# Optimization experiments

Measured on AMD Instinct MI355X. Metric: run time of the kernel, lower is better.

## Reference

```python
import jax, jax.numpy as jnp
import numpy as np

N_NODES = 20000
N_EDGES = 320000
F_IN = 256      # num_features_mol
HIDDEN = 512    # hidden_size


def _glorot(key, shape):
    fan_in, fan_out = shape
    lim = jnp.sqrt(6.0 / (fan_in + fan_out)).astype(jnp.float32)
    return jax.random.uniform(key, shape, jnp.float32, -lim, lim)


def setup_inputs() -> dict:
    key = jax.random.key(0)
    ks = jax.random.split(key, 12)
    x = jax.random.normal(ks[0], (N_NODES, F_IN), jnp.float32)
    edge_index = jax.random.randint(ks[1], (2, N_EDGES), 0, N_NODES, dtype=jnp.int64)
    d1, d2, d3 = F_IN * 2, F_IN * 2, F_IN * 4  # 512, 512, 1024
    return {
        "x": x,
        "edge_index": edge_index,
        # SAGEConv layer i: lin_l (neighbor, with bias), lin_r (root, no bias)
        "Wl1": _glorot(ks[2], (F_IN, d1)), "bl1": jnp.zeros((d1,), jnp.float32),
        "Wr1": _glorot(ks[3], (F_IN, d1)),
        "Wl2": _glorot(ks[4], (d1, d2)), "bl2": jnp.zeros((d2,), jnp.float32),
        "Wr2": _glorot(ks[5], (d1, d2)),
        "Wl3": _glorot(ks[6], (d2, d3)), "bl3": jnp.zeros((d3,), jnp.float32),
        "Wr3": _glorot(ks[7], (d2, d3)),
        # mol_fc_g1: Linear(4*F -> hidden)
        "Wfc": _glorot(ks[8], (d3, HIDDEN)), "bfc": jnp.zeros((HIDDEN,), jnp.float32),
    }


def _sage_mean(x, src, dst, Wl, bl, Wr):
    # mean-aggregate neighbor features: messages flow src -> dst
    msg = x[src]                                               # [E, d]
    agg = jax.ops.segment_sum(msg, dst, num_segments=N_NODES)  # [N, d]
    cnt = jax.ops.segment_sum(jnp.ones((src.shape[0],), x.dtype), dst,
                              num_segments=N_NODES)            # [N]
    mean = agg / jnp.maximum(cnt, 1.0)[:, None]                # zero-deg -> 0
    return mean @ Wl + bl + x @ Wr


def reference(x, edge_index, Wl1, bl1, Wr1, Wl2, bl2, Wr2, Wl3, bl3, Wr3, Wfc, bfc):
    src, dst = edge_index[0], edge_index[1]
    h = jax.nn.relu(_sage_mean(x, src, dst, Wl1, bl1, Wr1))
    h = jax.nn.relu(_sage_mean(h, src, dst, Wl2, bl2, Wr2))
    h = jax.nn.relu(_sage_mean(h, src, dst, Wl3, bl3, Wr3))
    return h @ Wfc + bfc                                       # [N, HIDDEN]
```

## Files before the change

kernel.cpp:

```cpp
#include <hip/hip_runtime.h>
#include <hip/hip_bf16.h>


typedef __bf16 bf16x8 __attribute__((ext_vector_type(8)));
typedef float  f32x4  __attribute__((ext_vector_type(4)));

#define N_NODES 20000
#define N_EDGES 320000
#define MPAD 20096

__device__ __forceinline__ int clampi(int v, int lo, int hi) {
    return v < lo ? lo : (v > hi ? hi : v);
}

__device__ __forceinline__ void load16_lds(const void* g, void* l) {
    __builtin_amdgcn_global_load_lds(
        (const __attribute__((address_space(1))) void*)g,
        (__attribute__((address_space(3))) void*)l, 16, 0, 0);
}


__global__ void k_count(const int* __restrict__ ei, int E, int* __restrict__ cnt) {
    int e = blockIdx.x * blockDim.x + threadIdx.x;
    if (e < E) atomicAdd(&cnt[clampi(ei[E + e], 0, N_NODES - 1)], 1);
}

__global__ __launch_bounds__(1024) void k_scan_block(const int* __restrict__ cnt,
                                                     int* __restrict__ off,
                                                     int* __restrict__ bsum, int n) {
    __shared__ int sm[1024];
    int b = blockIdx.x, tid = threadIdx.x;
    int i = b * 1024 + tid;
    int v = (i < n) ? cnt[i] : 0;
    sm[tid] = v;
    __syncthreads();
    for (int s = 1; s < 1024; s <<= 1) {
        int t = (tid >= s) ? sm[tid - s] : 0;
        __syncthreads();
        sm[tid] += t;
        __syncthreads();
    }
    if (i < n) off[i] = sm[tid] - v;
    if (tid == 1023) bsum[b] = sm[1023];
}

__global__ void k_scan_carry(const int* __restrict__ bsum, int* __restrict__ carry,
                             int nb, int* __restrict__ off, int n) {
    if (threadIdx.x == 0 && blockIdx.x == 0) {
        int acc = 0;
        for (int b = 0; b < nb; ++b) { carry[b] = acc; acc += bsum[b]; }
        off[n] = acc;
    }
}

__global__ __launch_bounds__(1024) void k_scan_add(int* __restrict__ off,
                                                   int* __restrict__ cur,
                                                   const int* __restrict__ carry, int n) {
    int i = blockIdx.x * 1024 + threadIdx.x;
    if (i < n) {
        int v = off[i] + carry[blockIdx.x];
        off[i] = v;
        cur[i] = v;
    }
}

__global__ void k_fill(const int* __restrict__ ei, int E,
                       int* __restrict__ cur, int* __restrict__ csr) {
    int e = blockIdx.x * blockDim.x + threadIdx.x;
    if (e < E) {
        int dst = clampi(ei[E + e], 0, N_NODES - 1);
        int src = clampi(ei[e], 0, N_NODES - 1);
        int pos = atomicAdd(&cur[dst], 1);
        if (pos >= 0 && pos < E) csr[pos] = src;
    }
}


struct TDesc { const float* W; __bf16* Wt; int K, N, KT, koff, tile0; };
struct TDescs { TDesc d[7]; };

__global__ void k_transpose_all(TDescs ds) {
    __shared__ float tile[32][33];
    int b = blockIdx.x;
    int di = 0;
#pragma unroll
    for (int i = 1; i < 7; ++i)
        if (b >= ds.d[i].tile0) di = i;
    const float* W = ds.d[di].W;
    __bf16* Wt = ds.d[di].Wt;
    int N = ds.d[di].N, KT = ds.d[di].KT, koff = ds.d[di].koff;
    int t = b - ds.d[di].tile0;
    int ntn = N >> 5;
    int nb = (t % ntn) * 32, kb = (t / ntn) * 32;
    for (int i = 0; i < 32; i += 8) {
        int k = kb + threadIdx.y + i, n = nb + threadIdx.x;
        tile[threadIdx.y + i][threadIdx.x] = W[(size_t)k * N + n];
    }
    __syncthreads();
    for (int i = 0; i < 32; i += 8) {
        int n = nb + threadIdx.y + i, k = koff + kb + threadIdx.x;
        size_t o = (size_t)(n >> 7) * ((size_t)KT * 128) + (size_t)(k >> 3) * 1024 +
                   (size_t)((n & 127) * 8) + (k & 7);
        Wt[o] = (__bf16)tile[threadIdx.x][threadIdx.y + i];
    }
}


__global__ __launch_bounds__(256) void k_x2bf(const float* __restrict__ x,
                                              __bf16* __restrict__ xrm,
                                              __bf16* __restrict__ acat) {
    int tid = threadIdx.x;
    int node = blockIdx.x * 8 + (tid >> 5);
    int f0 = (tid & 31) * 8;
    float4 u = *(const float4*)(x + (size_t)node * 256 + f0);
    float4 w = *(const float4*)(x + (size_t)node * 256 + f0 + 4);
    alignas(16) __bf16 tmp[8] = {(__bf16)u.x, (__bf16)u.y, (__bf16)u.z, (__bf16)u.w,
                                 (__bf16)w.x, (__bf16)w.y, (__bf16)w.z, (__bf16)w.w};
    *(uint4*)(xrm + (size_t)node * 256 + f0) = *(const uint4*)tmp;
    *(uint4*)(acat + (size_t)(node >> 7) * (512 * 128) +
              (size_t)(32 + (f0 >> 3)) * 1024 + (size_t)((node & 127) * 8)) =
        *(const uint4*)tmp;
}


template <int D, int KC>
__global__ __launch_bounds__(256) void k_agg(const __hip_bfloat16* __restrict__ hrm,
                                             const int* __restrict__ off,
                                             const int* __restrict__ csr,
                                             __bf16* __restrict__ acat) {
    constexpr int FPL = D / 64;
    int wave = threadIdx.x >> 6, lane = threadIdx.x & 63;
    int node = blockIdx.x * 4 + wave;
    int c0 = lane * FPL;
    int beg = off[node], end = off[node + 1];
    float a[FPL] = {};

    auto accum = [&](int s) {
        if constexpr (FPL == 8) {
            uint4 v = *(const uint4*)(hrm + (size_t)s * D + c0);
            const __hip_bfloat16* hb = (const __hip_bfloat16*)&v;
#pragma unroll
        for (int j = 0; j < 8; ++j) a[j] += __bfloat162float(hb[j]);
        } else {
            uint2 v = *(const uint2*)(hrm + (size_t)s * D + c0);
            const __hip_bfloat16* hb = (const __hip_bfloat16*)&v;
#pragma unroll
            for (int j = 0; j < 4; ++j) a[j] += __bfloat162float(hb[j]);
        }
    };

    int e = beg;
    for (; e + 1 < end; e += 2) {
        int s0 = csr[e], s1 = csr[e + 1];
        accum(s0);
        accum(s1);
    }
    if (e < end) accum(csr[e]);

    float inv = 1.f / fmaxf((float)(end - beg), 1.f);
    alignas(16) __bf16 tmp[FPL];
#pragma unroll
    for (int j = 0; j < FPL; ++j) tmp[j] = (__bf16)(a[j] * inv);

    __bf16* base = acat + (size_t)(node >> 7) * ((size_t)KC * 128) +
                   (size_t)((node & 127) * 8);
    if constexpr (FPL == 8) {
        *(uint4*)(base + (size_t)lane * 1024) = *(const uint4*)tmp;
    } else {
        *(uint2*)(base + (size_t)(lane >> 1) * 1024 + (size_t)((lane & 1) * 4)) =
            *(const uint2*)tmp;
    }
}


template <bool RELU, int OUTMODE>
__global__ __launch_bounds__(256) void k_gemm(const __bf16* __restrict__ A, int K, int M,
                                              const __bf16* __restrict__ B,
                                              const float* __restrict__ bias,
                                              __bf16* __restrict__ osw, int Kc, int coff,
                                              __bf16* __restrict__ orm, int ldrm,
                                              float* __restrict__ of32, int ldf,
                                              int rtiles, int ctlog2) {
    constexpr int SMEM = (OUTMODE == 2) ? 34816 : 32768;
    __shared__ char smem[SMEM];
    __bf16* Alds = (__bf16*)smem;
    __bf16* Blds = (__bf16*)(smem + 16384);

    int bid = blockIdx.x;
    int xcd = bid & 7, local = bid >> 3;
    int cmask = (1 << ctlog2) - 1;
    int colTile = local & cmask;
    int rowTile = (local >> ctlog2) * 8 + xcd;
    if (rowTile >= rtiles) return;

    const __bf16* Atile = A + (size_t)rowTile * ((size_t)K * 128);
    const __bf16* Btile = B + (size_t)colTile * ((size_t)K * 128);

    int tid = threadIdx.x;
    int wave = tid >> 6, lane = tid & 63;
    int wr = wave >> 1, wc = wave & 1;
    int quad = lane >> 4, l16 = lane & 15;

    f32x4 acc[4][4] = {};

    for (int k0 = 0; k0 < K; k0 += 64) {
        __syncthreads();
        const __bf16* gA = Atile + (size_t)k0 * 128;
        const __bf16* gB = Btile + (size_t)k0 * 128;
#pragma unroll
        for (int j = 0; j < 4; ++j) {
            int slot = (j * 256 + tid) * 8;
            load16_lds(gA + slot, Alds + slot);
            load16_lds(gB + slot, Blds + slot);
        }
        __syncthreads();
#pragma unroll
        for (int sp = 0; sp < 2; ++sp) {
            bf16x8 af[4], bf[4];
#pragma unroll
            for (int mi = 0; mi < 4; ++mi)
                af[mi] = *(const bf16x8*)(Alds + sp * 4096 + quad * 1024 +
                                          (wr * 64 + mi * 16 + l16) * 8);
#pragma unroll
            for (int ni = 0; ni < 4; ++ni)
                bf[ni] = *(const bf16x8*)(Blds + sp * 4096 + quad * 1024 +
                                          (wc * 64 + ni * 16 + l16) * 8);
#pragma unroll
            for (int mi = 0; mi < 4; ++mi)
#pragma unroll
                for (int ni = 0; ni < 4; ++ni)
                    acc[mi][ni] = __builtin_amdgcn_mfma_f32_16x16x32_bf16(
                        af[mi], bf[ni], acc[mi][ni], 0, 0, 0);
        }
    }

    int col0 = colTile * 128;
    int row0 = rowTile * 128;
    __syncthreads();

    if (OUTMODE != 2) {
        __bf16* cb = (__bf16*)smem;
#pragma unroll
        for (int ni = 0; ni < 4; ++ni) {
            int ct = wc * 64 + ni * 16 + l16;
            float bv = bias[col0 + ct];
#pragma unroll
            for (int mi = 0; mi < 4; ++mi) {
                int rb = wr * 64 + mi * 16 + quad * 4;
#pragma unroll
                for (int r = 0; r < 4; ++r) {
                    float v = acc[mi][ni][r] + bv;
                    if (RELU) v = fmaxf(v, 0.f);
                    cb[(ct >> 3) * 1024 + (rb + r) * 8 + (ct & 7)] = (__bf16)v;
                }
            }
        }
        __syncthreads();
        __bf16* dst = osw + (size_t)rowTile * ((size_t)Kc * 128) +
                      (size_t)((coff + col0) >> 3) * 1024;
#pragma unroll
        for (int p2 = 0; p2 < 8; ++p2) {
            int idx = (p2 * 256 + tid) * 8;
            *(uint4*)(dst + idx) = *(const uint4*)(cb + idx);
        }
        if (OUTMODE == 1) {
#pragma unroll
            for (int p2 = 0; p2 < 8; ++p2) {
                int rr = p2 * 16 + (tid >> 4);
                int cc = tid & 15;
                *(uint4*)(orm + (size_t)(row0 + rr) * ldrm + col0 + cc * 8) =
                    *(const uint4*)(cb + cc * 1024 + rr * 8);
            }
        }
    } else {
        float* cf = (float*)smem;
#pragma unroll
        for (int h = 0; h < 2; ++h) {
            if (wc == h) {
#pragma unroll
                for (int ni = 0; ni < 4; ++ni) {
                    int ctl = ni * 16 + l16;
                    float bv = bias[col0 + h * 64 + ctl];
#pragma unroll
                    for (int mi = 0; mi < 4; ++mi) {
                        int rb = wr * 64 + mi * 16 + quad * 4;
#pragma unroll
                        for (int r = 0; r < 4; ++r) {
                            float v = acc[mi][ni][r] + bv;
                            if (RELU) v = fmaxf(v, 0.f);
                            cf[(rb + r) * 68 + ctl] = v;
                        }
                    }
                }
            }
            __syncthreads();
            int chunk = tid & 15, rl = tid >> 4;
#pragma unroll
            for (int p2 = 0; p2 < 8; ++p2) {
                int rt = p2 * 16 + rl;
                int row = row0 + rt;
                if (row < M) {
                    float4 v = *(const float4*)(cf + rt * 68 + chunk * 4);
                    *(float4*)(of32 + (size_t)row * ldf + col0 + h * 64 + chunk * 4) = v;
                }
            }
            __syncthreads();
        }
    }
}


extern "C" void kernel_launch(void* const* d_in, const int* in_sizes, int n_in,
                              void* d_out, int out_size, void* d_ws, size_t ws_size,
                              hipStream_t stream) {
    const float* x   = (const float*)d_in[0];
    const int*   ei  = (const int*)d_in[1];
    const float* Wl1 = (const float*)d_in[2];
    const float* bl1 = (const float*)d_in[3];
    const float* Wr1 = (const float*)d_in[4];
    const float* Wl2 = (const float*)d_in[5];
    const float* bl2 = (const float*)d_in[6];
    const float* Wr2 = (const float*)d_in[7];
    const float* Wl3 = (const float*)d_in[8];
    const float* bl3 = (const float*)d_in[9];
    const float* Wr3 = (const float*)d_in[10];
    const float* Wfc = (const float*)d_in[11];
    const float* bfc = (const float*)d_in[12];
    float* out = (float*)d_out;

    const int NN = N_NODES, E = N_EDGES;
    const int NB = (NN + 1023) / 1024;

    char* p = (char*)d_ws;
    auto alloc = [&](size_t bytes) {
        char* r = p;
        p += (bytes + 511) & ~(size_t)511;
        return r;
    };
    int* cnt   = (int*)alloc((size_t)NN * 4);
    int* off   = (int*)alloc((size_t)(NN + 1) * 4);
    int* cur   = (int*)alloc((size_t)NN * 4);
    int* csr   = (int*)alloc((size_t)E * 4);
    int* bsum  = (int*)alloc((size_t)NB * 4);
    int* carry = (int*)alloc((size_t)NB * 4);
    __bf16* Acat1 = (__bf16*)alloc((size_t)MPAD * 512 * 2);
    __bf16* Acat2 = (__bf16*)alloc((size_t)MPAD * 1024 * 2);
    __bf16* Acat3 = (__bf16*)alloc((size_t)MPAD * 1024 * 2);
    __bf16* Hrm   = (__bf16*)alloc((size_t)MPAD * 512 * 2);
    __bf16* Xrm   = (__bf16*)alloc((size_t)MPAD * 256 * 2);
    __bf16* Wt1 = (__bf16*)alloc((size_t)512 * 512 * 2);
    __bf16* Wt2 = (__bf16*)alloc((size_t)512 * 1024 * 2);
    __bf16* Wt3 = (__bf16*)alloc((size_t)1024 * 1024 * 2);
    __bf16* Wt4 = (__bf16*)alloc((size_t)512 * 1024 * 2);
    __bf16* H3 = Acat2;

    k_x2bf<<<NN / 8, 256, 0, stream>>>(x, Xrm, Acat1);

    hipMemsetAsync(cnt, 0, (size_t)NN * 4, stream);
    k_count<<<(E + 255) / 256, 256, 0, stream>>>(ei, E, cnt);
    k_scan_block<<<NB, 1024, 0, stream>>>(cnt, off, bsum, NN);
    k_scan_carry<<<1, 64, 0, stream>>>(bsum, carry, NB, off, NN);
    k_scan_add<<<NB, 1024, 0, stream>>>(off, cur, carry, NN);
    k_fill<<<(E + 255) / 256, 256, 0, stream>>>(ei, E, cur, csr);

    TDescs td;
    td.d[0] = {Wl1, Wt1, 256, 512, 512, 0, 0};
    td.d[1] = {Wr1, Wt1, 256, 512, 512, 256, 128};
    td.d[2] = {Wl2, Wt2, 512, 512, 1024, 0, 256};
    td.d[3] = {Wr2, Wt2, 512, 512, 1024, 512, 512};
    td.d[4] = {Wl3, Wt3, 512, 1024, 1024, 0, 768};
    td.d[5] = {Wr3, Wt3, 512, 1024, 1024, 512, 1280};
    td.d[6] = {Wfc, Wt4, 1024, 512, 1024, 0, 1792};
    k_transpose_all<<<2304, dim3(32, 8), 0, stream>>>(td);

    int rtiles = (NN + 127) / 128;
    int rg = ((rtiles + 7) / 8) * 8;

    k_agg<256, 512><<<NN / 4, 256, 0, stream>>>(
        (const __hip_bfloat16*)Xrm, off, csr, Acat1);
    k_gemm<true, 1><<<rg * 4, 256, 0, stream>>>(
        Acat1, 512, NN, Wt1, bl1, Acat2, 1024, 512, Hrm, 512, nullptr, 0, rtiles, 2);

    k_agg<512, 1024><<<NN / 4, 256, 0, stream>>>(
        (const __hip_bfloat16*)Hrm, off, csr, Acat2);
    k_gemm<true, 1><<<rg * 4, 256, 0, stream>>>(
        Acat2, 1024, NN, Wt2, bl2, Acat3, 1024, 512, Hrm, 512, nullptr, 0, rtiles, 2);

    k_agg<512, 1024><<<NN / 4, 256, 0, stream>>>(
        (const __hip_bfloat16*)Hrm, off, csr, Acat3);
    k_gemm<true, 0><<<rg * 8, 256, 0, stream>>>(
        Acat3, 1024, NN, Wt3, bl3, H3, 1024, 0, nullptr, 0, nullptr, 0, rtiles, 3);

    k_gemm<false, 2><<<rg * 4, 256, 0, stream>>>(
        H3, 1024, NN, Wt4, bfc, nullptr, 0, 0, nullptr, 0, out, 512, rtiles, 2);
}
```

Before: 417.4 us.

## Fuse prep kernels into one launch, single-block scan, unroll aggregation by four

```diff
diff --git a/kernel.cpp b/kernel.cpp
--- a/kernel.cpp
+++ b/kernel.cpp
@@ -20,48 +20,82 @@
 }
 
 
-__global__ void k_count(const int* __restrict__ ei, int E, int* __restrict__ cnt) {
-    int e = blockIdx.x * blockDim.x + threadIdx.x;
-    if (e < E) atomicAdd(&cnt[clampi(ei[E + e], 0, N_NODES - 1)], 1);
-}
-
-__global__ __launch_bounds__(1024) void k_scan_block(const int* __restrict__ cnt,
-                                                     int* __restrict__ off,
-                                                     int* __restrict__ bsum, int n) {
+struct TDesc { const float* W; __bf16* Wt; int K, N, KT, koff, tile0; };
+struct TDescs { TDesc d[7]; };
+
+__global__ void k_prep(TDescs ds, const float* __restrict__ x,
+                       __bf16* __restrict__ xrm, __bf16* __restrict__ acat,
+                       const int* __restrict__ ei, int* __restrict__ cnt) {
+    __shared__ float tile[32][33];
+    int b = blockIdx.x;
+    int tid = threadIdx.y * 32 + threadIdx.x;
+
+    if (b < 2304) {
+        int di = 0;
+#pragma unroll
+        for (int i = 1; i < 7; ++i)
+            if (b >= ds.d[i].tile0) di = i;
+        const float* W = ds.d[di].W;
+        __bf16* Wt = ds.d[di].Wt;
+        int N = ds.d[di].N, KT = ds.d[di].KT, koff = ds.d[di].koff;
+        int t = b - ds.d[di].tile0;
+        int ntn = N >> 5;
+        int nb = (t % ntn) * 32, kb = (t / ntn) * 32;
+        for (int i = 0; i < 32; i += 8) {
+            int k = kb + threadIdx.y + i, n = nb + threadIdx.x;
+            tile[threadIdx.y + i][threadIdx.x] = W[(size_t)k * N + n];
+        }
+        __syncthreads();
+        for (int i = 0; i < 32; i += 8) {
+            int n = nb + threadIdx.y + i, k = koff + kb + threadIdx.x;
+            size_t o = (size_t)(n >> 7) * ((size_t)KT * 128) + (size_t)(k >> 3) * 1024 +
+                       (size_t)((n & 127) * 8) + (k & 7);
+            Wt[o] = (__bf16)tile[threadIdx.x][threadIdx.y + i];
+        }
+    } else if (b < 4804) {
+        int node = (b - 2304) * 8 + (tid >> 5);
+        int f0 = (tid & 31) * 8;
+        float4 u = *(const float4*)(x + (size_t)node * 256 + f0);
+        float4 w = *(const float4*)(x + (size_t)node * 256 + f0 + 4);
+        alignas(16) __bf16 tmp[8] = {(__bf16)u.x, (__bf16)u.y, (__bf16)u.z, (__bf16)u.w,
+                                     (__bf16)w.x, (__bf16)w.y, (__bf16)w.z, (__bf16)w.w};
+        *(uint4*)(xrm + (size_t)node * 256 + f0) = *(const uint4*)tmp;
+        *(uint4*)(acat + (size_t)(node >> 7) * (512 * 128) +
+                  (size_t)(32 + (f0 >> 3)) * 1024 + (size_t)((node & 127) * 8)) =
+            *(const uint4*)tmp;
+    } else {
+        int e = (b - 4804) * 256 + tid;
+        atomicAdd(&cnt[clampi(ei[N_EDGES + e], 0, N_NODES - 1)], 1);
+    }
+}
+
+
+__global__ __launch_bounds__(1024) void k_scan(const int* __restrict__ cnt,
+                                               int* __restrict__ off,
+                                               int* __restrict__ cur, int n) {
     __shared__ int sm[1024];
-    int b = blockIdx.x, tid = threadIdx.x;
-    int i = b * 1024 + tid;
-    int v = (i < n) ? cnt[i] : 0;
-    sm[tid] = v;
+    __shared__ int carry;
+    int tid = threadIdx.x;
+    if (tid == 0) carry = 0;
     __syncthreads();
-    for (int s = 1; s < 1024; s <<= 1) {
-        int t = (tid >= s) ? sm[tid - s] : 0;
-        __syncthreads();
-        sm[tid] += t;
-        __syncthreads();
-    }
-    if (i < n) off[i] = sm[tid] - v;
-    if (tid == 1023) bsum[b] = sm[1023];
-}
-
-__global__ void k_scan_carry(const int* __restrict__ bsum, int* __restrict__ carry,
-                             int nb, int* __restrict__ off, int n) {
-    if (threadIdx.x == 0 && blockIdx.x == 0) {
-        int acc = 0;
-        for (int b = 0; b < nb; ++b) { carry[b] = acc; acc += bsum[b]; }
-        off[n] = acc;
-    }
-}
-
-__global__ __launch_bounds__(1024) void k_scan_add(int* __restrict__ off,
-                                                   int* __restrict__ cur,
-                                                   const int* __restrict__ carry, int n) {
-    int i = blockIdx.x * 1024 + threadIdx.x;
-    if (i < n) {
-        int v = off[i] + carry[blockIdx.x];
-        off[i] = v;
-        cur[i] = v;
-    }
+    for (int base = 0; base < n; base += 1024) {
+        int i = base + tid;
+        int v = (i < n) ? cnt[i] : 0;
+        sm[tid] = v;
+        __syncthreads();
+        for (int s = 1; s < 1024; s <<= 1) {
+            int t = (tid >= s) ? sm[tid - s] : 0;
+            __syncthreads();
+            sm[tid] += t;
+            __syncthreads();
+        }
+        int exc = carry + sm[tid] - v;
+        if (i < n) { off[i] = exc; cur[i] = exc; }
+        __syncthreads();
+        if (tid == 1023) carry += sm[1023];
+        __syncthreads();
+    }
+    if (tid == 0) off[n] = carry;
 }
 
 __global__ void k_fill(const int* __restrict__ ei, int E,
@@ -73,53 +107,6 @@
         int pos = atomicAdd(&cur[dst], 1);
         if (pos >= 0 && pos < E) csr[pos] = src;
     }
-}
-
-
-struct TDesc { const float* W; __bf16* Wt; int K, N, KT, koff, tile0; };
-struct TDescs { TDesc d[7]; };
-
-__global__ void k_transpose_all(TDescs ds) {
-    __shared__ float tile[32][33];
-    int b = blockIdx.x;
-    int di = 0;
-#pragma unroll
-    for (int i = 1; i < 7; ++i)
-        if (b >= ds.d[i].tile0) di = i;
-    const float* W = ds.d[di].W;
-    __bf16* Wt = ds.d[di].Wt;
-    int N = ds.d[di].N, KT = ds.d[di].KT, koff = ds.d[di].koff;
-    int t = b - ds.d[di].tile0;
-    int ntn = N >> 5;
-    int nb = (t % ntn) * 32, kb = (t / ntn) * 32;
-    for (int i = 0; i < 32; i += 8) {
-        int k = kb + threadIdx.y + i, n = nb + threadIdx.x;
-        tile[threadIdx.y + i][threadIdx.x] = W[(size_t)k * N + n];
-    }
-    __syncthreads();
-    for (int i = 0; i < 32; i += 8) {
-        int n = nb + threadIdx.y + i, k = koff + kb + threadIdx.x;
-        size_t o = (size_t)(n >> 7) * ((size_t)KT * 128) + (size_t)(k >> 3) * 1024 +
-                   (size_t)((n & 127) * 8) + (k & 7);
-        Wt[o] = (__bf16)tile[threadIdx.x][threadIdx.y + i];
-    }
-}
-
-
-__global__ __launch_bounds__(256) void k_x2bf(const float* __restrict__ x,
-                                              __bf16* __restrict__ xrm,
-                                              __bf16* __restrict__ acat) {
-    int tid = threadIdx.x;
-    int node = blockIdx.x * 8 + (tid >> 5);
-    int f0 = (tid & 31) * 8;
-    float4 u = *(const float4*)(x + (size_t)node * 256 + f0);
-    float4 w = *(const float4*)(x + (size_t)node * 256 + f0 + 4);
-    alignas(16) __bf16 tmp[8] = {(__bf16)u.x, (__bf16)u.y, (__bf16)u.z, (__bf16)u.w,
-                                 (__bf16)w.x, (__bf16)w.y, (__bf16)w.z, (__bf16)w.w};
-    *(uint4*)(xrm + (size_t)node * 256 + f0) = *(const uint4*)tmp;
-    *(uint4*)(acat + (size_t)(node >> 7) * (512 * 128) +
-              (size_t)(32 + (f0 >> 3)) * 1024 + (size_t)((node & 127) * 8)) =
-        *(const uint4*)tmp;
 }
 
 
@@ -135,27 +122,35 @@
     int beg = off[node], end = off[node + 1];
     float a[FPL] = {};
 
-    auto accum = [&](int s) {
-        if constexpr (FPL == 8) {
-            uint4 v = *(const uint4*)(hrm + (size_t)s * D + c0);
+    if constexpr (FPL == 8) {
+        auto ldrow = [&](int s) { return *(const uint4*)(hrm + (size_t)s * D + c0); };
+        auto addv = [&](uint4 v) {
             const __hip_bfloat16* hb = (const __hip_bfloat16*)&v;
 #pragma unroll
-        for (int j = 0; j < 8; ++j) a[j] += __bfloat162float(hb[j]);
-        } else {
-            uint2 v = *(const uint2*)(hrm + (size_t)s * D + c0);
+            for (int j = 0; j < 8; ++j) a[j] += __bfloat162float(hb[j]);
+        };
+        int e = beg;
+        for (; e + 3 < end; e += 4) {
+            int s0 = csr[e], s1 = csr[e + 1], s2 = csr[e + 2], s3 = csr[e + 3];
+            uint4 v0 = ldrow(s0), v1 = ldrow(s1), v2 = ldrow(s2), v3 = ldrow(s3);
+            addv(v0); addv(v1); addv(v2); addv(v3);
+        }
+        for (; e < end; ++e) addv(ldrow(csr[e]));
+    } else {
+        auto ldrow = [&](int s) { return *(const uint2*)(hrm + (size_t)s * D + c0); };
+        auto addv = [&](uint2 v) {
             const __hip_bfloat16* hb = (const __hip_bfloat16*)&v;
 #pragma unroll
             for (int j = 0; j < 4; ++j) a[j] += __bfloat162float(hb[j]);
-        }
-    };
-
-    int e = beg;
-    for (; e + 1 < end; e += 2) {
-        int s0 = csr[e], s1 = csr[e + 1];
-        accum(s0);
-        accum(s1);
-    }
-    if (e < end) accum(csr[e]);
+        };
+        int e = beg;
+        for (; e + 3 < end; e += 4) {
+            int s0 = csr[e], s1 = csr[e + 1], s2 = csr[e + 2], s3 = csr[e + 3];
+            uint2 v0 = ldrow(s0), v1 = ldrow(s1), v2 = ldrow(s2), v3 = ldrow(s3);
+            addv(v0); addv(v1); addv(v2); addv(v3);
+        }
+        for (; e < end; ++e) addv(ldrow(csr[e]));
+    }
 
     float inv = 1.f / fmaxf((float)(end - beg), 1.f);
     alignas(16) __bf16 tmp[FPL];
@@ -329,7 +324,6 @@
     float* out = (float*)d_out;
 
     const int NN = N_NODES, E = N_EDGES;
-    const int NB = (NN + 1023) / 1024;
 
     char* p = (char*)d_ws;
     auto alloc = [&](size_t bytes) {
@@ -341,8 +335,6 @@
     int* off   = (int*)alloc((size_t)(NN + 1) * 4);
     int* cur   = (int*)alloc((size_t)NN * 4);
     int* csr   = (int*)alloc((size_t)E * 4);
-    int* bsum  = (int*)alloc((size_t)NB * 4);
-    int* carry = (int*)alloc((size_t)NB * 4);
     __bf16* Acat1 = (__bf16*)alloc((size_t)MPAD * 512 * 2);
     __bf16* Acat2 = (__bf16*)alloc((size_t)MPAD * 1024 * 2);
     __bf16* Acat3 = (__bf16*)alloc((size_t)MPAD * 1024 * 2);
@@ -354,15 +346,7 @@
     __bf16* Wt4 = (__bf16*)alloc((size_t)512 * 1024 * 2);
     __bf16* H3 = Acat2;
 
-    k_x2bf<<<NN / 8, 256, 0, stream>>>(x, Xrm, Acat1);
-
     hipMemsetAsync(cnt, 0, (size_t)NN * 4, stream);
-    k_count<<<(E + 255) / 256, 256, 0, stream>>>(ei, E, cnt);
-    k_scan_block<<<NB, 1024, 0, stream>>>(cnt, off, bsum, NN);
-    k_scan_carry<<<1, 64, 0, stream>>>(bsum, carry, NB, off, NN);
-    k_scan_add<<<NB, 1024, 0, stream>>>(off, cur, carry, NN);
-    k_fill<<<(E + 255) / 256, 256, 0, stream>>>(ei, E, cur, csr);
-
     TDescs td;
     td.d[0] = {Wl1, Wt1, 256, 512, 512, 0, 0};
     td.d[1] = {Wr1, Wt1, 256, 512, 512, 256, 128};
@@ -371,7 +355,10 @@
     td.d[4] = {Wl3, Wt3, 512, 1024, 1024, 0, 768};
     td.d[5] = {Wr3, Wt3, 512, 1024, 1024, 512, 1280};
     td.d[6] = {Wfc, Wt4, 1024, 512, 1024, 0, 1792};
-    k_transpose_all<<<2304, dim3(32, 8), 0, stream>>>(td);
+    k_prep<<<6054, dim3(32, 8), 0, stream>>>(td, x, Xrm, Acat1, ei, cnt);
+
+    k_scan<<<1, 1024, 0, stream>>>(cnt, off, cur, NN);
+    k_fill<<<(E + 255) / 256, 256, 0, stream>>>(ei, E, cur, csr);
 
     int rtiles = (NN + 127) / 128;
     int rg = ((rtiles + 7) / 8) * 8;
```

Result: slower. 443.4 us (+6.2%).
